# Kernel optimization log

Measured on AMD Instinct MI355X. Metric: run time of the kernel, lower is better.

The kernel has to match this reference:

```python
import jax, jax.numpy as jnp
import numpy as np

BETA = 0.25
N_E = 8192
E_DIM = 64
B, L = 32, 512


def setup_inputs() -> dict:
    key = jax.random.key(0)
    k1, k2, k3 = jax.random.split(key, 3)
    z = jax.random.normal(k1, (B, E_DIM, L), dtype=jnp.float32)
    mask = jax.random.randint(k2, (B, L), 0, 2, dtype=jnp.int32)
    # nn.Embedding init: uniform(-1/n_e, 1/n_e)
    emb = jax.random.uniform(k3, (N_E, E_DIM), dtype=jnp.float32,
                             minval=-1.0 / N_E, maxval=1.0 / N_E)
    return {"z": z, "mask": mask, "emb": emb}


def reference(z, mask, emb):
    sg = jax.lax.stop_gradient
    b, c, l = z.shape            # c == e_dim
    n_e = emb.shape[0]
    zt = jnp.transpose(z, (0, 2, 1))          # (B, L, C)
    zf = zt.reshape(-1, c)                    # (B*L, C)
    m = mask.reshape(-1, 1).astype(zf.dtype)  # (B*L, 1) per-token mask

    # pairwise squared distances (with masked z, as in original)
    zm = zf * m
    d = (jnp.sum(zf * zf * m, axis=1, keepdims=True)
         + jnp.sum(emb * emb, axis=1)
         - 2.0 * jnp.matmul(zm, emb.T))       # (B*L, n_e)

    idx = jnp.argmin(d, axis=1)               # (B*L,)
    min_encodings = jax.nn.one_hot(idx, n_e, dtype=zf.dtype)  # (B*L, n_e)
    z_q = emb[idx].reshape(zt.shape)          # gather == one_hot @ emb

    # masked MSE losses (mask broadcast over the C dim, mean over mask.sum()*C)
    m3 = m.reshape(b, l, 1)
    denom = jnp.sum(m3) * c
    embedding_loss = jnp.sum((sg(z_q) - zt) ** 2 * m3) / denom
    commitment_loss = jnp.sum((z_q - sg(zt)) ** 2 * m3) / denom
    loss = embedding_loss + BETA * commitment_loss

    # straight-through estimator
    z_q_st = zt + sg(z_q - zt)

    e_mean = jnp.mean(min_encodings, axis=0)
    perplexity = jnp.exp(-jnp.sum(e_mean * jnp.log(e_mean + 1e-10)))

    z_q_out = jnp.transpose(z_q_st, (0, 2, 1))  # back to (B, C, L)
    return loss, z_q_out, perplexity, min_encodings, idx[:, None]
```

## Files before the change

### kernel.cpp

```cpp
#include <hip/hip_runtime.h>
#include <cstdint>
#include <cstddef>

#define TOK 16384
#define NE  8192
#define CD  64

#define O_ZQ   1
#define O_PERP 1048577
#define O_ENC  1048578
#define O_IDX  135266306

__global__ __launch_bounds__(256) void k_init(
    const float* __restrict__ z, const int* __restrict__ mask,
    const float* __restrict__ emb,
    unsigned long long* __restrict__ packed,
    float* __restrict__ s_z, float* __restrict__ s_e,
    int* __restrict__ hist) {
  int g = blockIdx.x * 256 + threadIdx.x;
  if (g < TOK) {
    int t = g, b = t >> 9, l = t & 511;
    const float* zp = z + (size_t)b * 32768 + l;
    float r[8];
#pragma unroll
    for (int j = 0; j < 8; ++j) { float v = zp[(size_t)j * 512]; r[j] = __fmul_rn(v, v); }
#pragma unroll
    for (int i = 8; i < 64; i += 8)
#pragma unroll
      for (int j = 0; j < 8; ++j) { float v = zp[(size_t)(i + j) * 512]; r[j] = __fadd_rn(r[j], __fmul_rn(v, v)); }
    float s = __fadd_rn(__fadd_rn(__fadd_rn(r[0], r[1]), __fadd_rn(r[2], r[3])),
                        __fadd_rn(__fadd_rn(r[4], r[5]), __fadd_rn(r[6], r[7])));
    s_z[t] = mask[t] ? s : 0.0f;
    packed[t] = ~0ull;
  } else if (g < TOK + NE) {
    int i = g - TOK;
    const float* ep = emb + (size_t)i * 64;
    float r[8];
#pragma unroll
    for (int j = 0; j < 8; ++j) { float v = ep[j]; r[j] = __fmul_rn(v, v); }
#pragma unroll
    for (int kk = 8; kk < 64; kk += 8)
#pragma unroll
      for (int j = 0; j < 8; ++j) { float v = ep[kk + j]; r[j] = __fadd_rn(r[j], __fmul_rn(v, v)); }
    float s = __fadd_rn(__fadd_rn(__fadd_rn(r[0], r[1]), __fadd_rn(r[2], r[3])),
                        __fadd_rn(__fadd_rn(r[4], r[5]), __fadd_rn(r[6], r[7])));
    s_e[i] = s;
    hist[i] = 0;
  }
}

__global__ __launch_bounds__(256) void k_search(
    const float* __restrict__ z, const int* __restrict__ mask,
    const float* __restrict__ emb,
    const float* __restrict__ s_z, const float* __restrict__ s_e,
    unsigned long long* __restrict__ packed,
    float* __restrict__ enc_out) {
  __shared__ __align__(16) float zs[64][68];
  __shared__ __align__(16) float es[128][68];

  const int tid = threadIdx.x;
  const int I0 = blockIdx.x * 128;
  const int T0 = blockIdx.y * 64;
  const int b  = T0 >> 9;
  const int l0 = T0 & 511;

  {
    const float4 z4 = make_float4(0.f, 0.f, 0.f, 0.f);
    float* base = enc_out + (size_t)T0 * 8192 + I0;
#pragma unroll
    for (int r = 0; r < 8; ++r) {
      int id  = r * 256 + tid;
      int row = id >> 5;
      int c4  = id & 31;
      *(float4*)(base + (size_t)row * 8192 + c4 * 4) = z4;
    }
  }

  {
    int lq = tid & 63;
    int m  = mask[T0 + lq];
#pragma unroll
    for (int rep = 0; rep < 16; ++rep) {
      int c = (tid >> 6) + rep * 4;
      float v = z[(size_t)b * 32768 + (size_t)c * 512 + l0 + lq];
      zs[lq][c] = m ? v : 0.0f;
    }
  }
  {
    int cq = tid & 63;
#pragma unroll
    for (int rep = 0; rep < 32; ++rep) {
      int i = (tid >> 6) + rep * 4;
      es[i][cq] = emb[(size_t)(I0 + i) * 64 + cq];
    }
  }
  __syncthreads();

  const int ty = tid >> 4;
  const int tx = tid & 15;

  float acc[4][8];
#pragma unroll
  for (int m = 0; m < 4; ++m)
#pragma unroll
    for (int j = 0; j < 8; ++j) acc[m][j] = 0.0f;

#pragma unroll 2
  for (int k = 0; k < 64; k += 4) {
    float4 zv[4], ev[8];
#pragma unroll
    for (int m = 0; m < 4; ++m) zv[m] = *(const float4*)&zs[ty * 4 + m][k];
#pragma unroll
    for (int j = 0; j < 8; ++j) ev[j] = *(const float4*)&es[tx + 16 * j][k];
#pragma unroll
    for (int m = 0; m < 4; ++m)
#pragma unroll
      for (int j = 0; j < 8; ++j) {
        acc[m][j] = fmaf(zv[m].x, ev[j].x, acc[m][j]);
        acc[m][j] = fmaf(zv[m].y, ev[j].y, acc[m][j]);
        acc[m][j] = fmaf(zv[m].z, ev[j].z, acc[m][j]);
        acc[m][j] = fmaf(zv[m].w, ev[j].w, acc[m][j]);
      }
  }

  float szv[4];
#pragma unroll
  for (int m = 0; m < 4; ++m) szv[m] = s_z[T0 + ty * 4 + m];

  unsigned long long best[4] = {~0ull, ~0ull, ~0ull, ~0ull};
#pragma unroll
  for (int j = 0; j < 8; ++j) {
    int i = I0 + tx + 16 * j;
    float se = s_e[i];
#pragma unroll
    for (int m = 0; m < 4; ++m) {
      float c1 = __fadd_rn(szv[m], se);
      float d  = __fsub_rn(c1, __fmul_rn(2.0f, acc[m][j]));
      unsigned int db = __float_as_uint(d);
      db = ((int)db < 0) ? ~db : (db | 0x80000000u);
      unsigned long long p = ((unsigned long long)db << 32) | (unsigned int)i;
      best[m] = (p < best[m]) ? p : best[m];
    }
  }

  __syncthreads();
  unsigned long long* red = reinterpret_cast<unsigned long long*>(&zs[0][0]);
#pragma unroll
  for (int m = 0; m < 4; ++m) red[(ty * 4 + m) * 16 + tx] = best[m];
  __syncthreads();

  if (tid < 64) {
    unsigned long long bb = red[tid * 16];
#pragma unroll
    for (int x = 1; x < 16; ++x) {
      unsigned long long q = red[tid * 16 + x];
      bb = (q < bb) ? q : bb;
    }
    atomicMin(&packed[T0 + tid], bb);
  }
}

__global__ __launch_bounds__(256) void k_finalize(
    const float* __restrict__ z, const int* __restrict__ mask,
    const float* __restrict__ emb,
    const unsigned long long* __restrict__ packed,
    float* __restrict__ out_zq, float* __restrict__ out_enc,
    float* __restrict__ out_idx,
    int* __restrict__ hist, float* __restrict__ token_loss) {
  int t    = blockIdx.x * 4 + (threadIdx.x >> 6);
  int lane = threadIdx.x & 63;
  unsigned long long p = packed[t];
  int idx = (int)(unsigned int)(p & 0xFFFFFFFFu);
  int b = t >> 9, l = t & 511;

  float e  = emb[(size_t)idx * 64 + lane];
  float zv = z[(size_t)b * 32768 + (size_t)lane * 512 + l];
  out_zq[(size_t)b * 32768 + (size_t)lane * 512 + l] = __fadd_rn(zv, __fsub_rn(e, zv));

  float dterm = __fsub_rn(e, zv);
  float sq = __fmul_rn(dterm, dterm);
#pragma unroll
  for (int off = 32; off; off >>= 1) sq += __shfl_xor(sq, off, 64);

  if (lane == 0) {
    token_loss[t] = mask[t] ? sq : 0.0f;
    atomicAdd(&hist[idx], 1);
    out_idx[t] = (float)idx;
    out_enc[(size_t)t * 8192 + idx] = 1.0f;
  }
}

__global__ __launch_bounds__(256) void k_scalars(
    const float* __restrict__ token_loss, const int* __restrict__ mask,
    const int* __restrict__ hist, float* __restrict__ out) {
  __shared__ float sf[256];
  __shared__ int   si[256];
  __shared__ float sh[256];
  int tid = threadIdx.x;
  float s = 0.f, h = 0.f;
  int ms = 0;
  for (int i = tid; i < TOK; i += 256) { s += token_loss[i]; ms += mask[i]; }
  for (int i = tid; i < NE; i += 256) {
    float pm = (float)hist[i] * (1.0f / 16384.0f);
    h += pm * logf(pm + 1e-10f);
  }
  sf[tid] = s; si[tid] = ms; sh[tid] = h;
  __syncthreads();
  for (int off = 128; off; off >>= 1) {
    if (tid < off) { sf[tid] += sf[tid + off]; si[tid] += si[tid + off]; sh[tid] += sh[tid + off]; }
    __syncthreads();
  }
  if (tid == 0) {
    float denom = (float)(si[0] * 64);
    float el = sf[0] / denom;
    out[0]      = __fadd_rn(el, __fmul_rn(0.25f, el));
    out[O_PERP] = expf(-sh[0]);
  }
}

extern "C" void kernel_launch(void* const* d_in, const int* in_sizes, int n_in,
                              void* d_out, int out_size, void* d_ws, size_t ws_size,
                              hipStream_t stream) {
  const float* z    = (const float*)d_in[0];
  const int*   mask = (const int*)d_in[1];
  const float* emb  = (const float*)d_in[2];
  float* out = (float*)d_out;
  char*  ws  = (char*)d_ws;

  unsigned long long* packed = (unsigned long long*)ws;
  float* s_z        = (float*)(ws + 131072);
  float* s_e        = (float*)(ws + 196608);
  int*   hist       = (int*)  (ws + 229376);
  float* token_loss = (float*)(ws + 262144);

  k_init<<<96, 256, 0, stream>>>(z, mask, emb, packed, s_z, s_e, hist);

  dim3 g1(64, 256, 1);
  k_search<<<g1, 256, 0, stream>>>(z, mask, emb, s_z, s_e, packed, out + O_ENC);

  k_finalize<<<4096, 256, 0, stream>>>(z, mask, emb, packed,
                                       out + O_ZQ, out + O_ENC, out + O_IDX,
                                       hist, token_loss);

  k_scalars<<<1, 256, 0, stream>>>(token_loss, mask, hist, out);
}
```

Measured before the change: 386.8 us.

## Reorder search prologue and restructure finalize for coalesced z access

```diff
diff --git a/kernel.cpp b/kernel.cpp
--- a/kernel.cpp
+++ b/kernel.cpp
@@ -65,6 +65,26 @@
   const int l0 = T0 & 511;
 
   {
+    int lq = tid & 63;
+    int m  = mask[T0 + lq];
+#pragma unroll
+    for (int rep = 0; rep < 16; ++rep) {
+      int c = (tid >> 6) + rep * 4;
+      float v = z[(size_t)b * 32768 + (size_t)c * 512 + l0 + lq];
+      zs[lq][c] = m ? v : 0.0f;
+    }
+  }
+  {
+    int cq = tid & 63;
+#pragma unroll
+    for (int rep = 0; rep < 32; ++rep) {
+      int i = (tid >> 6) + rep * 4;
+      es[i][cq] = emb[(size_t)(I0 + i) * 64 + cq];
+    }
+  }
+  __syncthreads();
+
+  {
     const float4 z4 = make_float4(0.f, 0.f, 0.f, 0.f);
     float* base = enc_out + (size_t)T0 * 8192 + I0;
 #pragma unroll
@@ -76,28 +96,14 @@
     }
   }
 
-  {
-    int lq = tid & 63;
-    int m  = mask[T0 + lq];
-#pragma unroll
-    for (int rep = 0; rep < 16; ++rep) {
-      int c = (tid >> 6) + rep * 4;
-      float v = z[(size_t)b * 32768 + (size_t)c * 512 + l0 + lq];
-      zs[lq][c] = m ? v : 0.0f;
-    }
-  }
-  {
-    int cq = tid & 63;
-#pragma unroll
-    for (int rep = 0; rep < 32; ++rep) {
-      int i = (tid >> 6) + rep * 4;
-      es[i][cq] = emb[(size_t)(I0 + i) * 64 + cq];
-    }
-  }
-  __syncthreads();
-
   const int ty = tid >> 4;
   const int tx = tid & 15;
+
+  float szv[4], sev[8];
+#pragma unroll
+  for (int m = 0; m < 4; ++m) szv[m] = s_z[T0 + ty * 4 + m];
+#pragma unroll
+  for (int j = 0; j < 8; ++j) sev[j] = s_e[I0 + tx + 16 * j];
 
   float acc[4][8];
 #pragma unroll
@@ -123,18 +129,13 @@
       }
   }
 
-  float szv[4];
-#pragma unroll
-  for (int m = 0; m < 4; ++m) szv[m] = s_z[T0 + ty * 4 + m];
-
   unsigned long long best[4] = {~0ull, ~0ull, ~0ull, ~0ull};
 #pragma unroll
   for (int j = 0; j < 8; ++j) {
     int i = I0 + tx + 16 * j;
-    float se = s_e[i];
 #pragma unroll
     for (int m = 0; m < 4; ++m) {
-      float c1 = __fadd_rn(szv[m], se);
+      float c1 = __fadd_rn(szv[m], sev[j]);
       float d  = __fsub_rn(c1, __fmul_rn(2.0f, acc[m][j]));
       unsigned int db = __float_as_uint(d);
       db = ((int)db < 0) ? ~db : (db | 0x80000000u);
@@ -160,33 +161,49 @@
   }
 }
 
-__global__ __launch_bounds__(256) void k_finalize(
+__global__ __launch_bounds__(512) void k_finalize(
     const float* __restrict__ z, const int* __restrict__ mask,
     const float* __restrict__ emb,
     const unsigned long long* __restrict__ packed,
     float* __restrict__ out_zq, float* __restrict__ out_enc,
     float* __restrict__ out_idx,
     int* __restrict__ hist, float* __restrict__ token_loss) {
-  int t    = blockIdx.x * 4 + (threadIdx.x >> 6);
-  int lane = threadIdx.x & 63;
-  unsigned long long p = packed[t];
-  int idx = (int)(unsigned int)(p & 0xFFFFFFFFu);
-  int b = t >> 9, l = t & 511;
-
-  float e  = emb[(size_t)idx * 64 + lane];
-  float zv = z[(size_t)b * 32768 + (size_t)lane * 512 + l];
-  out_zq[(size_t)b * 32768 + (size_t)lane * 512 + l] = __fadd_rn(zv, __fsub_rn(e, zv));
-
-  float dterm = __fsub_rn(e, zv);
-  float sq = __fmul_rn(dterm, dterm);
-#pragma unroll
-  for (int off = 32; off; off >>= 1) sq += __shfl_xor(sq, off, 64);
-
-  if (lane == 0) {
-    token_loss[t] = mask[t] ? sq : 0.0f;
-    atomicAdd(&hist[idx], 1);
+  __shared__ float part[8][64];
+  const int T0   = blockIdx.x * 64;
+  const int lane = threadIdx.x & 63;
+  const int w    = threadIdx.x >> 6;
+  const int b    = T0 >> 9;
+  const int l0   = T0 & 511;
+  const int t    = T0 + lane;
+
+  const int idx = (int)(unsigned int)(packed[t] & 0xFFFFFFFFu);
+
+  const float* zb = z      + (size_t)b * 32768 + l0 + lane;
+  float*       qb = out_zq + (size_t)b * 32768 + l0 + lane;
+
+  float sq = 0.0f;
+#pragma unroll
+  for (int cc = 0; cc < 8; ++cc) {
+    int c = w * 8 + cc;
+    float zv   = zb[(size_t)c * 512];
+    float e    = emb[(size_t)idx * 64 + c];
+    float diff = __fsub_rn(e, zv);
+    qb[(size_t)c * 512] = __fadd_rn(zv, diff);
+    sq = fmaf(diff, diff, sq);
+  }
+  part[w][lane] = sq;
+  __syncthreads();
+
+  if (w == 0) {
+    float s = __fadd_rn(
+        __fadd_rn(__fadd_rn(part[0][lane], part[1][lane]),
+                  __fadd_rn(part[2][lane], part[3][lane])),
+        __fadd_rn(__fadd_rn(part[4][lane], part[5][lane]),
+                  __fadd_rn(part[6][lane], part[7][lane])));
+    token_loss[t] = mask[t] ? s : 0.0f;
     out_idx[t] = (float)idx;
     out_enc[(size_t)t * 8192 + idx] = 1.0f;
+    atomicAdd(&hist[idx], 1);
   }
 }
 
@@ -238,9 +255,9 @@
   dim3 g1(64, 256, 1);
   k_search<<<g1, 256, 0, stream>>>(z, mask, emb, s_z, s_e, packed, out + O_ENC);
 
-  k_finalize<<<4096, 256, 0, stream>>>(z, mask, emb, packed,
-                                       out + O_ZQ, out + O_ENC, out + O_IDX,
-                                       hist, token_loss);
+  k_finalize<<<256, 512, 0, stream>>>(z, mask, emb, packed,
+                                      out + O_ZQ, out + O_ENC, out + O_IDX,
+                                      hist, token_loss);
 
   k_scalars<<<1, 256, 0, stream>>>(token_loss, mask, hist, out);
 }
```

Result: no change. 385.1 us (-0.4%).
